# Optimization experiments

Hardware: AMD Instinct MI355X
Metric: run time of the kernel (lower is better)

## Reference

```python
import jax, jax.numpy as jnp
import numpy as np

N, E, IN, H, L = 100000, 1600000, 128, 64, 3


def setup_inputs() -> dict:
    key = jax.random.key(0)
    ks = jax.random.split(key, 4)
    x = jax.random.normal(ks[0], (N, IN), dtype=jnp.float32)
    edge_index = jax.random.randint(ks[1], (2, E), 0, N, dtype=jnp.int32)
    enc_w = jax.random.normal(ks[2], (IN, H), dtype=jnp.float32) * 0.05
    enc_b = jnp.zeros((H,), jnp.float32)
    conv_w = jax.random.normal(ks[3], (L, H, H), dtype=jnp.float32) * 0.05
    conv_b = jnp.zeros((L, H), jnp.float32)
    return {"x": x, "edge_index": edge_index, "enc_w": enc_w, "enc_b": enc_b,
            "conv_w": conv_w, "conv_b": conv_b}


def _nuc(m):
    # nuclear norm of [N, C] via eigvals of the small C x C Gram matrix
    g = m.T @ m
    ev = jnp.linalg.eigvalsh(g)
    return jnp.sum(jnp.sqrt(jnp.clip(ev, 0.0, None)))


def _rank_diff(x):
    xn = x / _nuc(x)
    i = jnp.argmax(jnp.sum(jnp.abs(xn), axis=1))
    j = jnp.argmax(jnp.sum(jnp.abs(xn), axis=0))
    m0 = jnp.take(xn, i, axis=0)[None, :]   # [1, C]
    m1 = jnp.take(xn, j, axis=1)[:, None]   # [N, 1]
    m0 = jnp.where(jnp.take(m0[0], j) < 0.0, -m0, m0)
    xh = m1 @ m0
    xh = xh / _nuc(xh)
    return _nuc(xn - xh)


def _dirichlet(x, src, dst, deg, rw):
    # edges (src, dst) already include self loops; deg = degree(src)
    xn = x / jnp.linalg.norm(x)
    if rw:
        d = xn[src] - xn[dst]
        e = jnp.sum(d * d)
    else:
        xs = xn * jax.lax.rsqrt(deg)[:, None]
        d = xs[src] - xs[dst]
        coef = jax.lax.rsqrt(deg[src] * deg[dst])
        e = jnp.sum(coef * jnp.sum(d * d, axis=1))
    return 0.5 * e


def reference(x, edge_index, enc_w, enc_b, conv_w, conv_b):
    n = x.shape[0]
    loops = jnp.arange(n, dtype=edge_index.dtype)
    src = jnp.concatenate([edge_index[0], loops])
    dst = jnp.concatenate([edge_index[1], loops])
    ones = jnp.ones(src.shape[0], x.dtype)
    deg_dst = jax.ops.segment_sum(ones, dst, num_segments=n)   # GCN norm degree
    dis = jax.lax.rsqrt(deg_dst)
    norm = dis[src] * dis[dst]
    deg_src = jax.ops.segment_sum(ones, src, num_segments=n)   # dirichlet degree

    h = x @ enc_w + enc_b                                      # encoder
    energies = [_dirichlet(jax.lax.stop_gradient(h), src, dst, deg_src, rw=False)]
    energies_sym = []
    ranks = []
    for i in range(L):
        # GCNConv: linear -> gather -> sym-normalized scatter-add -> bias
        xw = h @ conv_w[i]
        msg = xw[src] * norm[:, None]
        h = jax.ops.segment_sum(msg, dst, num_segments=n) + conv_b[i]
        h = jax.nn.relu(h)
        hs = jax.lax.stop_gradient(h)
        energies.append(_dirichlet(hs, src, dst, deg_src, rw=True))
        energies_sym.append(_dirichlet(hs, src, dst, deg_src, rw=False))
        ranks.append(_rank_diff(hs))
    return h, jnp.stack(energies), jnp.stack(energies_sym), jnp.stack(ranks)
```

## Files before the change

### kernel.cpp

```cpp
#include <hip/hip_runtime.h>

#define WF 64

__device__ inline float wredsum(float v) {
#pragma unroll
  for (int m = 32; m; m >>= 1) v += __shfl_xor(v, m, WF);
  return v;
}
__device__ inline float4 wredsum4(float4 v) {
#pragma unroll
  for (int m = 32; m; m >>= 1) {
    v.x += __shfl_xor(v.x, m, WF);
    v.y += __shfl_xor(v.y, m, WF);
    v.z += __shfl_xor(v.z, m, WF);
    v.w += __shfl_xor(v.w, m, WF);
  }
  return v;
}
__device__ inline float wredmin(float v) {
#pragma unroll
  for (int m = 32; m; m >>= 1) v = fminf(v, __shfl_xor(v, m, WF));
  return v;
}
__device__ inline float wredmax(float v) {
#pragma unroll
  for (int m = 32; m; m >>= 1) v = fmaxf(v, __shfl_xor(v, m, WF));
  return v;
}

__device__ inline float fastrcp(float x) {
  float r;
  asm("v_rcp_f32 %0, %1" : "=v"(r) : "v"(x));
  return r;
}

__device__ inline void atomAddF(float* p, float v) { unsafeAtomicAdd(p, v); }

__global__ __launch_bounds__(256) void k_init(int* degs, int* degd, float* G,
                                              float* colsum, float* scal, int n) {
  int i = blockIdx.x * 256 + threadIdx.x;
  if (i < n) { degs[i] = 1; degd[i] = 1; }
  if (i < 3 * 4096) G[i] = 0.f;
  if (i < 3 * 64) colsum[i] = 0.f;
  if (i < 64) scal[i] = 0.f;
}

__global__ __launch_bounds__(256) void k_deg(const int* src, const int* dst,
                                             int* degs, int* degd, int e) {
  int i = blockIdx.x * 256 + threadIdx.x;
  int stride = gridDim.x * 256;
  for (; i < e; i += stride) {
    atomicAdd(&degs[src[i]], 1);
    atomicAdd(&degd[dst[i]], 1);
  }
}

__global__ __launch_bounds__(256) void k_nodescal(const int* degs, const int* degd,
                                                  float4* cn4, float* degsum, int n) {
  int i = blockIdx.x * 256 + threadIdx.x;
  if (i < n) {
    float fs = (float)degs[i], fd = (float)degd[i];
    float rs_ = rsqrtf(fs);
    float4 v;
    v.x = rsqrtf(fd);
    v.y = 1.f / fs;
    v.z = rs_;
    v.w = rs_ * rs_ * rs_;
    cn4[i] = v;
    degsum[i] = fs + fd;
  }
}

__global__ __launch_bounds__(256) void k_scan1(const int* degd, int* start, int* bsum, int n) {
  __shared__ int sb[256];
  int t = threadIdx.x, i = blockIdx.x * 256 + t;
  int v = (i < n) ? degd[i] : 0;
  sb[t] = v;
  __syncthreads();
  for (int off = 1; off < 256; off <<= 1) {
    int add = (t >= off) ? sb[t - off] : 0;
    __syncthreads();
    sb[t] += add;
    __syncthreads();
  }
  if (i < n) start[i] = sb[t] - v;
  if (t == 255) bsum[blockIdx.x] = sb[255];
}

__global__ __launch_bounds__(512) void k_scan2(int* bsum, int nb) {
  __shared__ int sb[512];
  int t = threadIdx.x;
  int v = (t < nb) ? bsum[t] : 0;
  sb[t] = v;
  __syncthreads();
  for (int off = 1; off < 512; off <<= 1) {
    int add = (t >= off) ? sb[t - off] : 0;
    __syncthreads();
    sb[t] += add;
    __syncthreads();
  }
  if (t < nb) bsum[t] = sb[t] - v;
}

__global__ __launch_bounds__(256) void k_scan3(int* start, const int* bsum, int* cursor,
                                               int n, int total) {
  int i = blockIdx.x * 256 + threadIdx.x;
  if (i < n) {
    int v = start[i] + bsum[i >> 8];
    start[i] = v;
    cursor[i] = v;
  }
  if (i == 0) start[n] = total;
}

__global__ __launch_bounds__(256) void k_scatter(const int* src, const int* dst, int* cursor,
                                                 int* csr, int e, int n) {
  int i = blockIdx.x * 256 + threadIdx.x;
  int tot = e + n;
  if (i >= tot) return;
  int s, d;
  if (i < e) { s = src[i]; d = dst[i]; } else { s = i - e; d = i - e; }
  int pos = atomicAdd(&cursor[d], 1);
  csr[pos] = s;
}

__global__ __launch_bounds__(256) void k_enc(const float* __restrict__ x,
                                             const float* __restrict__ W,
                                             const float* __restrict__ b,
                                             const float4* __restrict__ cn4,
                                             float* __restrict__ X,
                                             float* __restrict__ nsq,
                                             float4* __restrict__ P, int n) {
  __shared__ float Wl[128 * 64];
  for (int idx = threadIdx.x; idx < 128 * 64; idx += 256) Wl[idx] = W[idx];
  __syncthreads();
  int w = threadIdx.x >> 6, c = threadIdx.x & 63;
  float bc = b[c];
  for (int node = blockIdx.x * 4 + w; node < n; node += gridDim.x * 4) {
    const float4* xr4 = (const float4*)(x + (size_t)node * 128);
    float acc = bc;
#pragma unroll
    for (int k4 = 0; k4 < 32; k4++) {
      float4 xv = xr4[k4];
      acc += xv.x * Wl[(k4 * 4 + 0) * 64 + c];
      acc += xv.y * Wl[(k4 * 4 + 1) * 64 + c];
      acc += xv.z * Wl[(k4 * 4 + 2) * 64 + c];
      acc += xv.w * Wl[(k4 * 4 + 3) * 64 + c];
    }
    X[(size_t)node * 64 + c] = acc;
    float r = wredsum(acc * acc);
    if (c == 0) {
      nsq[node] = r;
      float4 c4 = cn4[node];
      P[node] = make_float4(c4.x, c4.y, c4.z, r * c4.w);
    }
  }
}

template <int AGGC>
__device__ inline void gather4(const float* __restrict__ H, const float4* __restrict__ P,
                               const int* __restrict__ csr, int k0, int k1, int g, int l16,
                               float4& agg0, float4& agg1, float4& aggC,
                               float& su, float& sv) {
  int kk = k0 + g;
  int last = k1 - 1;
  int s0 = csr[min(kk, last)];
  int s1 = csr[min(kk + 4, last)];
  int s2 = csr[min(kk + 8, last)];
  int s3 = csr[min(kk + 12, last)];
  while (kk < k1) {
    int kn = kk + 16;
    float4 h0 = *(const float4*)(H + (size_t)s0 * 64 + 4 * l16);
    float4 h1 = *(const float4*)(H + (size_t)s1 * 64 + 4 * l16);
    float4 h2 = *(const float4*)(H + (size_t)s2 * 64 + 4 * l16);
    float4 h3 = *(const float4*)(H + (size_t)s3 * 64 + 4 * l16);
    float4 Q0 = P[s0], Q1 = P[s1], Q2 = P[s2], Q3 = P[s3];
    s0 = csr[min(kn, last)];
    s1 = csr[min(kn + 4, last)];
    s2 = csr[min(kn + 8, last)];
    s3 = csr[min(kn + 12, last)];
    float m1 = (kk + 4 < k1) ? 1.f : 0.f;
    float m2 = (kk + 8 < k1) ? 1.f : 0.f;
    float m3 = (kk + 12 < k1) ? 1.f : 0.f;
    agg0.x += h0.x; agg0.y += h0.y; agg0.z += h0.z; agg0.w += h0.w;
    agg1.x = fmaf(h0.x, Q0.y, agg1.x); agg1.y = fmaf(h0.y, Q0.y, agg1.y);
    agg1.z = fmaf(h0.z, Q0.y, agg1.z); agg1.w = fmaf(h0.w, Q0.y, agg1.w);
    if (AGGC) {
      aggC.x = fmaf(h0.x, Q0.x, aggC.x); aggC.y = fmaf(h0.y, Q0.x, aggC.y);
      aggC.z = fmaf(h0.z, Q0.x, aggC.z); aggC.w = fmaf(h0.w, Q0.x, aggC.w);
    }
    su += Q0.w; sv += Q0.z;
    {
      float y = Q1.y * m1;
      agg0.x = fmaf(h1.x, m1, agg0.x); agg0.y = fmaf(h1.y, m1, agg0.y);
      agg0.z = fmaf(h1.z, m1, agg0.z); agg0.w = fmaf(h1.w, m1, agg0.w);
      agg1.x = fmaf(h1.x, y, agg1.x); agg1.y = fmaf(h1.y, y, agg1.y);
      agg1.z = fmaf(h1.z, y, agg1.z); agg1.w = fmaf(h1.w, y, agg1.w);
      if (AGGC) {
        float xq = Q1.x * m1;
        aggC.x = fmaf(h1.x, xq, aggC.x); aggC.y = fmaf(h1.y, xq, aggC.y);
        aggC.z = fmaf(h1.z, xq, aggC.z); aggC.w = fmaf(h1.w, xq, aggC.w);
      }
      su = fmaf(Q1.w, m1, su); sv = fmaf(Q1.z, m1, sv);
    }
    {
      float y = Q2.y * m2;
      agg0.x = fmaf(h2.x, m2, agg0.x); agg0.y = fmaf(h2.y, m2, agg0.y);
      agg0.z = fmaf(h2.z, m2, agg0.z); agg0.w = fmaf(h2.w, m2, agg0.w);
      agg1.x = fmaf(h2.x, y, agg1.x); agg1.y = fmaf(h2.y, y, agg1.y);
      agg1.z = fmaf(h2.z, y, agg1.z); agg1.w = fmaf(h2.w, y, agg1.w);
      if (AGGC) {
        float xq = Q2.x * m2;
        aggC.x = fmaf(h2.x, xq, aggC.x); aggC.y = fmaf(h2.y, xq, aggC.y);
        aggC.z = fmaf(h2.z, xq, aggC.z); aggC.w = fmaf(h2.w, xq, aggC.w);
      }
      su = fmaf(Q2.w, m2, su); sv = fmaf(Q2.z, m2, sv);
    }
    {
      float y = Q3.y * m3;
      agg0.x = fmaf(h3.x, m3, agg0.x); agg0.y = fmaf(h3.y, m3, agg0.y);
      agg0.z = fmaf(h3.z, m3, agg0.z); agg0.w = fmaf(h3.w, m3, agg0.w);
      agg1.x = fmaf(h3.x, y, agg1.x); agg1.y = fmaf(h3.y, y, agg1.y);
      agg1.z = fmaf(h3.z, y, agg1.z); agg1.w = fmaf(h3.w, y, agg1.w);
      if (AGGC) {
        float xq = Q3.x * m3;
        aggC.x = fmaf(h3.x, xq, aggC.x); aggC.y = fmaf(h3.y, xq, aggC.y);
        aggC.z = fmaf(h3.z, xq, aggC.z); aggC.w = fmaf(h3.w, xq, aggC.w);
      }
      su = fmaf(Q3.w, m3, su); sv = fmaf(Q3.z, m3, sv);
    }
    kk = kn;
  }
}

__global__ __launch_bounds__(256) void k_convpass(
    const float* __restrict__ H, const float4* __restrict__ P,
    const float* __restrict__ nsq, const float* __restrict__ degsum,
    const float4* __restrict__ cn4, const int* __restrict__ start,
    const int* __restrict__ csr, const float* __restrict__ W,
    const float* __restrict__ bias, float* __restrict__ T,
    float4* __restrict__ Pn, float* __restrict__ nsqN,
    float* __restrict__ scal5, float* __restrict__ G, float* __restrict__ colsum,
    float* __restrict__ bmv, int* __restrict__ bmi, int n) {
  __shared__ float Wl[4096];
  __shared__ float rowbuf[4][64];
  __shared__ float red[4][5];
  __shared__ float colred[4][64];
  __shared__ float mvs[4];
  __shared__ int mis[4];
  int t = threadIdx.x, w = t >> 6, lane = t & 63, g = lane >> 4, l16 = lane & 15;
  for (int i = t; i < 4096; i += 256) Wl[i] = W[i];
  __syncthreads();
  float a0 = 0.f, a1 = 0.f, a2 = 0.f, a3 = 0.f, a4 = 0.f;
  float Greg[16];
#pragma unroll
  for (int k = 0; k < 16; k++) Greg[k] = 0.f;
  float cacc = 0.f, best = -1.f;
  int bi = 0;
  float bc = bias[lane];
  int wid = blockIdx.x * 4 + w, nw = gridDim.x * 4;
  int iters = (n + nw - 1) / nw;
  for (int it = 0; it < iters; it++) {
    int d = wid + it * nw;
    bool valid = d < n;
    float tv = 0.f;
    if (valid) {
      int k0 = start[d], k1 = start[d + 1];
      float4 hd = *(const float4*)(H + (size_t)d * 64 + 4 * l16);
      float4 pd = P[d];
      float nqd = nsq[d];
      float dsum = degsum[d];
      float4 agg0 = {0.f, 0.f, 0.f, 0.f};
      float4 agg1 = {0.f, 0.f, 0.f, 0.f};
      float4 aggC = {0.f, 0.f, 0.f, 0.f};
      float su = 0.f, sv = 0.f;
      gather4<1>(H, P, csr, k0, k1, g, l16, agg0, agg1, aggC, su, sv);
      float td0 = agg0.x * hd.x + agg0.y * hd.y + agg0.z * hd.z + agg0.w * hd.w;
      float td1 = agg1.x * hd.x + agg1.y * hd.y + agg1.z * hd.z + agg1.w * hd.w;
      float4 r4 = wredsum4(make_float4(td0, td1, su, sv));
      float dot1 = r4.x, dot2 = r4.y;
      su = r4.z * 0.0625f;
      sv = r4.w * 0.0625f;
      a0 += dsum * nqd;
      a1 += dot1;
      a2 += pd.z * su + pd.w * sv;
      a3 += pd.y * dot2;
      a4 += nqd;
      aggC.x += __shfl_xor(aggC.x, 16); aggC.y += __shfl_xor(aggC.y, 16);
      aggC.z += __shfl_xor(aggC.z, 16); aggC.w += __shfl_xor(aggC.w, 16);
      aggC.x += __shfl_xor(aggC.x, 32); aggC.y += __shfl_xor(aggC.y, 32);
      aggC.z += __shfl_xor(aggC.z, 32); aggC.w += __shfl_xor(aggC.w, 32);
      float mv = 0.f;
#pragma unroll
      for (int kq = 0; kq < 16; kq++) {
        float ax = __shfl(aggC.x, kq, 16);
        float ay = __shfl(aggC.y, kq, 16);
        float az = __shfl(aggC.z, kq, 16);
        float aw = __shfl(aggC.w, kq, 16);
        mv += ax * Wl[(4 * kq + 0) * 64 + lane];
        mv += ay * Wl[(4 * kq + 1) * 64 + lane];
        mv += az * Wl[(4 * kq + 2) * 64 + lane];
        mv += aw * Wl[(4 * kq + 3) * 64 + lane];
      }
      tv = fmaxf(fmaf(pd.x, mv, bc), 0.f);
      T[(size_t)d * 64 + lane] = tv;
      float r = wredsum(tv * tv);
      float atv = fabsf(tv);
      cacc += atv;
      float rsum = wredsum(atv);
      if (rsum > best) { best = rsum; bi = d; }
      if (lane == 0) {
        nsqN[d] = r;
        float4 c4 = cn4[d];
        Pn[d] = make_float4(c4.x, c4.y, c4.z, r * c4.w);
      }
    }
    rowbuf[w][lane] = tv;
    __syncthreads();
#pragma unroll
    for (int rr = 0; rr < 4; rr++) {
      float hj = rowbuf[rr][lane];
#pragma unroll
      for (int k = 0; k < 16; k++) Greg[k] = fmaf(rowbuf[rr][w + 4 * k], hj, Greg[k]);
    }
    __syncthreads();
  }
#pragma unroll
  for (int k = 0; k < 16; k++) atomAddF(&G[(w + 4 * k) * 64 + lane], Greg[k]);
  colred[w][lane] = cacc;
  if (lane == 0) {
    red[w][0] = a0; red[w][1] = a1; red[w][2] = a2; red[w][3] = a3; red[w][4] = a4;
    mvs[w] = best; mis[w] = bi;
  }
  __syncthreads();
  if (t < 64) {
    float cs = colred[0][t] + colred[1][t] + colred[2][t] + colred[3][t];
    atomAddF(&colsum[t], cs);
  }
  if (t == 0) {
#pragma unroll
    for (int j = 0; j < 5; j++)
      atomAddF(&scal5[j], red[0][j] + red[1][j] + red[2][j] + red[3][j]);
    float bv = mvs[0]; int bix = mis[0];
    for (int q = 1; q < 4; q++)
      if (mvs[q] > bv || (mvs[q] == bv && mis[q] < bix)) { bv = mvs[q]; bix = mis[q]; }
    bmv[blockIdx.x] = bv;
    bmi[blockIdx.x] = bix;
  }
}

__global__ __launch_bounds__(64) void k_finalize(const float* T, const float* bmv,
                                                 const int* bmi, int nblocks,
                                                 const float* colsum, float* rowslot,
                                                 int* jstar, int n) {
  int t = threadIdx.x;
  float bv = -1.f;
  int bix = 0x7fffffff;
  for (int b = t; b < nblocks; b += 64) {
    float v = bmv[b]; int ix = bmi[b];
    if (v > bv || (v == bv && ix < bix)) { bv = v; bix = ix; }
  }
#pragma unroll
  for (int m = 32; m; m >>= 1) {
    float ov = __shfl_xor(bv, m); int oi = __shfl_xor(bix, m);
    if (ov > bv || (ov == bv && oi < bix)) { bv = ov; bix = oi; }
  }
  float cv = colsum[t];
  int cj = t;
#pragma unroll
  for (int m = 32; m; m >>= 1) {
    float ov = __shfl_xor(cv, m); int oj = __shfl_xor(cj, m);
    if (ov > cv || (ov == cv && oj < cj)) { cv = ov; cj = oj; }
  }
  if (t == 0) jstar[0] = cj;
  rowslot[t] = T[(size_t)bix * 64 + t];
}

__device__ float tridiag_sumsqrt(float (*A)[65], float* vbuf, float* wbuf,
                                 float (*wpart)[64], float2* de, float* esh, int t) {
  bool w0 = (t < 64);
  int lane = t & 63, w4 = t >> 6;
  for (int k = 0; k < 62; k++) {
    float beta = 0.f;
    if (w0) {
      float acol = A[t][k];
      float xs = (t >= k + 2) ? acol : 0.f;
      float sigma = wredsum(xs * xs);
      float x1 = __shfl(acol, k + 1, WF);
      float alpha = -copysignf(sqrtf(fmaf(x1, x1, sigma)), x1);
      float v1 = x1 - alpha;
      float vv = fmaf(v1, v1, sigma);
      beta = (vv > 1e-37f) ? 2.f / vv : 0.f;
      vbuf[t] = (t == k + 1) ? v1 : xs;
      if (t == 0) esh[k] = alpha;
    }
    __syncthreads();
    {
      float s0 = 0.f, s1 = 0.f, s2 = 0.f, s3 = 0.f;
#pragma unroll
      for (int i2 = 0; i2 < 4; i2++) {
        int j = w4 + 16 * i2;
        s0 = fmaf(A[lane][j], vbuf[j], s0);
        s1 = fmaf(A[lane][j + 4], vbuf[j + 4], s1);
        s2 = fmaf(A[lane][j + 8], vbuf[j + 8], s2);
        s3 = fmaf(A[lane][j + 12], vbuf[j + 12], s3);
      }
      wpart[w4][lane] = (s0 + s1) + (s2 + s3);
    }
    __syncthreads();
    if (w0) {
      float p = beta * (wpart[0][t] + wpart[1][t] + wpart[2][t] + wpart[3][t]);
      float dot = wredsum(vbuf[t] * p);
      float K = 0.5f * beta * dot;
      wbuf[t] = fmaf(-K, vbuf[t], p);
    }
    __syncthreads();
    {
      float vj = vbuf[lane], wj = wbuf[lane];
#pragma unroll
      for (int i2 = 0; i2 < 16; i2++) {
        int i = w4 + 4 * i2;
        A[i][lane] -= vbuf[i] * wj + wbuf[i] * vj;
      }
    }
    __syncthreads();
  }
  if (t == 0) { esh[62] = A[63][62]; esh[63] = 0.f; }
  __syncthreads();
  float gmin = 0.f, gmax = 0.f;
  if (w0) {
    float dt = A[t][t];
    float ep = (t >= 1) ? esh[t - 1] : 0.f;
    float en = (t <= 62) ? esh[t] : 0.f;
    de[t] = make_float2(dt, ep * ep);
    float rad = fabsf(ep) + fabsf(en);
    gmin = wredmin(dt - rad);
    gmax = wredmax(dt + rad);
  }
  __syncthreads();
  float lam = 0.f;
  if (w0) {
    float range = gmax - gmin;
    float lo = gmin - 1e-3f * range - 1e-30f;
    float hi = gmax + 1e-3f * range + 1e-30f;
    for (int it = 0; it < 30; it++) {
      float mid = 0.5f * (lo + hi);
      float q = de[0].x - mid;
      int cnt = (q < 0.f) ? 1 : 0;
      for (int i = 1; i < 64; i++) {
        float2 dc = de[i];
        float qq = (dc.x - mid) - dc.y * fastrcp(q);
        q = (fabsf(qq) < 1e-30f) ? -1e-30f : qq;
        cnt += (q < 0.f) ? 1 : 0;
      }
      if (cnt > t) hi = mid; else lo = mid;
    }
    lam = 0.5f * (lo + hi);
  }
  float svv = w0 ? sqrtf(fmaxf(lam, 0.f)) : 0.f;
  return wredsum(svv);
}

__global__ __launch_bounds__(256, 4) void k_final(
    const float* __restrict__ H, const float4* __restrict__ P,
    const float* __restrict__ nsq, const float* __restrict__ degsum,
    const int* __restrict__ start, const int* __restrict__ csr,
    float* __restrict__ scal5, const float* __restrict__ Gbase,
    const float* __restrict__ rowslot, const int* __restrict__ jstar,
    float* __restrict__ rankOut, int n, int nbE) {
  __shared__ float A[64][65];
  __shared__ float vbuf[64], wbuf[64], esh[64];
  __shared__ float wpart[4][64];
  __shared__ float2 de[64];
  __shared__ float u[64], m0[64];
  __shared__ float shn;
  __shared__ float red[4][5];
  int t = threadIdx.x, w = t >> 6, lane = t & 63, g = lane >> 4, l16 = lane & 15;
  if (blockIdx.x < 3) {
    int l = blockIdx.x;
    const float* Gl = Gbase + l * 4096;
    for (int idx = t; idx < 4096; idx += 256) A[idx >> 6][idx & 63] = Gl[idx];
    __syncthreads();
    float nuc1 = tridiag_sumsqrt(A, vbuf, wbuf, wpart, de, esh, t);
    if (t == 0) shn = nuc1;
    __syncthreads();
    float s = 1.f / shn;
    int js = jstar[l];
    if (t < 64) {
      float rv = rowslot[l * 64 + t];
      float rn2 = wredsum(rv * rv);
      float sign = (rowslot[l * 64 + js] < 0.f) ? -1.f : 1.f;
      m0[t] = sign * rv * rsqrtf(rn2);
      u[t] = s * Gl[t * 64 + js] * rsqrtf(Gl[js * 64 + js]);
    }
    __syncthreads();
    float s2 = s * s;
    for (int idx = t; idx < 4096; idx += 256) {
      int i = idx >> 6, j = idx & 63;
      A[i][j] = s2 * Gl[idx] - u[i] * m0[j] - m0[i] * u[j] + m0[i] * m0[j];
    }
    __syncthreads();
    float nuc2 = tridiag_sumsqrt(A, vbuf, wbuf, wpart, de, esh, t);
    if (t == 0) rankOut[l] = nuc2;
    return;
  }
  float a0 = 0.f, a1 = 0.f, a2 = 0.f, a3 = 0.f, a4 = 0.f;
  int wid = (blockIdx.x - 3) * 4 + w, nw = nbE * 4;
  for (int d = wid; d < n; d += nw) {
    int k0 = start[d], k1 = start[d + 1];
    float4 hd = *(const float4*)(H + (size_t)d * 64 + 4 * l16);
    float4 pd = P[d];
    float nqd = nsq[d];
    float dsum = degsum[d];
    float4 agg0 = {0.f, 0.f, 0.f, 0.f};
    float4 agg1 = {0.f, 0.f, 0.f, 0.f};
    float4 aggC = {0.f, 0.f, 0.f, 0.f};
    float su = 0.f, sv = 0.f;
    gather4<0>(H, P, csr, k0, k1, g, l16, agg0, agg1, aggC, su, sv);
    float td0 = agg0.x * hd.x + agg0.y * hd.y + agg0.z * hd.z + agg0.w * hd.w;
    float td1 = agg1.x * hd.x + agg1.y * hd.y + agg1.z * hd.z + agg1.w * hd.w;
    float4 r4 = wredsum4(make_float4(td0, td1, su, sv));
    a0 += dsum * nqd;
    a1 += r4.x;
    a2 += pd.z * (r4.z * 0.0625f) + pd.w * (r4.w * 0.0625f);
    a3 += pd.y * r4.y;
    a4 += nqd;
  }
  if (lane == 0) {
    red[w][0] = a0; red[w][1] = a1; red[w][2] = a2; red[w][3] = a3; red[w][4] = a4;
  }
  __syncthreads();
  if (t == 0) {
#pragma unroll
    for (int j = 0; j < 5; j++)
      atomAddF(&scal5[j], red[0][j] + red[1][j] + red[2][j] + red[3][j]);
  }
}

__global__ __launch_bounds__(64) void k_epi(const float* scal, float* outsc) {
  if (threadIdx.x == 0) {
    for (int st = 0; st < 4; st++) {
      const float* a = scal + 5 * st;
      float inv = 1.f / a[4];
      float rw = 0.5f * (a[0] - 2.f * a[1]) * inv;
      float sym = 0.5f * (a[2] - 2.f * a[3]) * inv;
      if (st == 0) outsc[0] = sym;
      else { outsc[st] = rw; outsc[3 + st] = sym; }
    }
    for (int l = 0; l < 3; l++) outsc[7 + l] = scal[20 + l];
  }
}

extern "C" void kernel_launch(void* const* d_in, const int* in_sizes, int n_in,
                              void* d_out, int out_size, void* d_ws, size_t ws_size,
                              hipStream_t stream) {
  const float* x      = (const float*)d_in[0];
  const int*   ei     = (const int*)d_in[1];
  const float* enc_w  = (const float*)d_in[2];
  const float* enc_b  = (const float*)d_in[3];
  const float* conv_w = (const float*)d_in[4];
  const float* conv_b = (const float*)d_in[5];
  const int n = in_sizes[0] / 128;
  const int e = in_sizes[1] / 2;
  const int* src = ei;
  const int* dst = ei + e;
  float* OUT = (float*)d_out;
  float* outsc = OUT + (size_t)n * 64;

  char* p = (char*)d_ws;
  auto alloc = [&](size_t bytes) -> char* {
    char* r = p;
    p += (bytes + 255) & ~size_t(255);
    return r;
  };
  float*  X      = (float*)alloc((size_t)n * 64 * 4);
  float*  Yf     = (float*)alloc((size_t)n * 64 * 4);
  int*    csr    = (int*)alloc((size_t)(e + n) * 4);
  int*    degs   = (int*)alloc((size_t)n * 4);
  int*    degd   = (int*)alloc((size_t)n * 4);
  float4* cn4    = (float4*)alloc((size_t)n * 16);
  float*  degsum = (float*)alloc((size_t)n * 4);
  int*    start  = (int*)alloc((size_t)(n + 1) * 4);
  int*    cursor = (int*)alloc((size_t)n * 4);
  int*    bsum   = (int*)alloc(4096);
  float*  nsqA   = (float*)alloc((size_t)n * 4);
  float*  nsqB   = (float*)alloc((size_t)n * 4);
  float4* Pa     = (float4*)alloc((size_t)n * 16);
  float4* Pb     = (float4*)alloc((size_t)n * 16);
  float*  G      = (float*)alloc(3 * 4096 * 4);
  float*  colsum = (float*)alloc(3 * 64 * 4);
  float*  bmv    = (float*)alloc(2048 * 4);
  int*    bmi    = (int*)alloc(2048 * 4);
  float*  rowslot= (float*)alloc(3 * 64 * 4);
  float*  scal   = (float*)alloc(64 * 4);
  int*    ij     = (int*)alloc(64 * 4);

  int nb = (n + 255) / 256;
  const int NBL = 2048;

  k_init<<<nb, 256, 0, stream>>>(degs, degd, G, colsum, scal, n);
  k_deg<<<2048, 256, 0, stream>>>(src, dst, degs, degd, e);
  k_nodescal<<<nb, 256, 0, stream>>>(degs, degd, cn4, degsum, n);
  k_scan1<<<nb, 256, 0, stream>>>(degd, start, bsum, n);
  k_scan2<<<1, 512, 0, stream>>>(bsum, nb);
  k_scan3<<<nb, 256, 0, stream>>>(start, bsum, cursor, n, e + n);
  k_scatter<<<(e + n + 255) / 256, 256, 0, stream>>>(src, dst, cursor, csr, e, n);
  k_enc<<<NBL, 256, 0, stream>>>(x, enc_w, enc_b, cn4, X, nsqA, Pa, n);

  k_convpass<<<NBL, 256, 0, stream>>>(X, Pa, nsqA, degsum, cn4, start, csr,
                                      conv_w, conv_b, Yf, Pb, nsqB,
                                      scal, G, colsum, bmv, bmi, n);
  k_finalize<<<1, 64, 0, stream>>>(Yf, bmv, bmi, NBL, colsum, rowslot, ij, n);

  k_convpass<<<NBL, 256, 0, stream>>>(Yf, Pb, nsqB, degsum, cn4, start, csr,
                                      conv_w + 4096, conv_b + 64, X, Pa, nsqA,
                                      scal + 5, G + 4096, colsum + 64, bmv, bmi, n);
  k_finalize<<<1, 64, 0, stream>>>(X, bmv, bmi, NBL, colsum + 64, rowslot + 64, ij + 1, n);

  k_convpass<<<NBL, 256, 0, stream>>>(X, Pa, nsqA, degsum, cn4, start, csr,
                                      conv_w + 2 * 4096, conv_b + 128, OUT, Pb, nsqB,
                                      scal + 10, G + 2 * 4096, colsum + 128, bmv, bmi, n);
  k_finalize<<<1, 64, 0, stream>>>(OUT, bmv, bmi, NBL, colsum + 128, rowslot + 128, ij + 2, n);

  k_final<<<NBL + 3, 256, 0, stream>>>(OUT, Pb, nsqB, degsum, start, csr,
                                       scal + 15, G, rowslot, ij, scal + 20, n, NBL);
  k_epi<<<1, 64, 0, stream>>>(scal, outsc);
}
```

Measured before the change: 1.435 ms.

## Gather neighbor features in bf16, shrink per-node scalars, overlap rank solves with conv passes

```diff
diff --git a/kernel.cpp b/kernel.cpp
--- a/kernel.cpp
+++ b/kernel.cpp
@@ -35,6 +35,36 @@
 }
 
 __device__ inline void atomAddF(float* p, float v) { unsafeAtomicAdd(p, v); }
+
+__device__ inline unsigned short f2bf(float f) {
+  unsigned u = __float_as_uint(f);
+  unsigned r = u + 0x7FFFu + ((u >> 16) & 1u);
+  return (unsigned short)(r >> 16);
+}
+__device__ inline float bf2f(unsigned short h) {
+  return __uint_as_float(((unsigned)h) << 16);
+}
+
+struct ConvS {
+  float Wl[4096];
+  float rowbuf[4][64];
+  float red[4][5];
+  float colred[4][64];
+  float mvs[4];
+  int mis[4];
+};
+struct RankS {
+  float A[64][65];
+  float vbuf[64], wbuf[64], esh[64];
+  float wpart[4][64];
+  float2 de[64];
+  float u[64], m0[64];
+  float shn;
+};
+union SmemU {
+  ConvS c;
+  RankS r;
+};
 
 __global__ __launch_bounds__(256) void k_init(int* degs, int* degd, float* G,
                                               float* colsum, float* scal, int n) {
@@ -56,17 +86,11 @@
 }
 
 __global__ __launch_bounds__(256) void k_nodescal(const int* degs, const int* degd,
-                                                  float4* cn4, float* degsum, int n) {
+                                                  float2* Pf, float* degsum, int n) {
   int i = blockIdx.x * 256 + threadIdx.x;
   if (i < n) {
     float fs = (float)degs[i], fd = (float)degd[i];
-    float rs_ = rsqrtf(fs);
-    float4 v;
-    v.x = rsqrtf(fd);
-    v.y = 1.f / fs;
-    v.z = rs_;
-    v.w = rs_ * rs_ * rs_;
-    cn4[i] = v;
+    Pf[i] = make_float2(rsqrtf(fd), rsqrtf(fs));
     degsum[i] = fs + fd;
   }
 }
@@ -127,10 +151,9 @@
 __global__ __launch_bounds__(256) void k_enc(const float* __restrict__ x,
                                              const float* __restrict__ W,
                                              const float* __restrict__ b,
-                                             const float4* __restrict__ cn4,
                                              float* __restrict__ X,
-                                             float* __restrict__ nsq,
-                                             float4* __restrict__ P, int n) {
+                                             unsigned short* __restrict__ Xb,
+                                             float* __restrict__ nsq, int n) {
   __shared__ float Wl[128 * 64];
   for (int idx = threadIdx.x; idx < 128 * 64; idx += 256) Wl[idx] = W[idx];
   __syncthreads();
@@ -148,17 +171,15 @@
       acc += xv.w * Wl[(k4 * 4 + 3) * 64 + c];
     }
     X[(size_t)node * 64 + c] = acc;
+    Xb[(size_t)node * 64 + c] = f2bf(acc);
     float r = wredsum(acc * acc);
-    if (c == 0) {
-      nsq[node] = r;
-      float4 c4 = cn4[node];
-      P[node] = make_float4(c4.x, c4.y, c4.z, r * c4.w);
-    }
+    if (c == 0) nsq[node] = r;
   }
 }
 
 template <int AGGC>
-__device__ inline void gather4(const float* __restrict__ H, const float4* __restrict__ P,
+__device__ inline void gatherB(const unsigned short* __restrict__ Hb,
+                               const float2* __restrict__ Pf,
                                const int* __restrict__ csr, int k0, int k1, int g, int l16,
                                float4& agg0, float4& agg1, float4& aggC,
                                float& su, float& sv) {
@@ -170,11 +191,11 @@
   int s3 = csr[min(kk + 12, last)];
   while (kk < k1) {
     int kn = kk + 16;
-    float4 h0 = *(const float4*)(H + (size_t)s0 * 64 + 4 * l16);
-    float4 h1 = *(const float4*)(H + (size_t)s1 * 64 + 4 * l16);
-    float4 h2 = *(const float4*)(H + (size_t)s2 * 64 + 4 * l16);
-    float4 h3 = *(const float4*)(H + (size_t)s3 * 64 + 4 * l16);
-    float4 Q0 = P[s0], Q1 = P[s1], Q2 = P[s2], Q3 = P[s3];
+    ushort4 b0 = *(const ushort4*)(Hb + (size_t)s0 * 64 + 4 * l16);
+    ushort4 b1 = *(const ushort4*)(Hb + (size_t)s1 * 64 + 4 * l16);
+    ushort4 b2 = *(const ushort4*)(Hb + (size_t)s2 * 64 + 4 * l16);
+    ushort4 b3 = *(const ushort4*)(Hb + (size_t)s3 * 64 + 4 * l16);
+    float2 p0 = Pf[s0], p1 = Pf[s1], p2 = Pf[s2], p3 = Pf[s3];
     s0 = csr[min(kn, last)];
     s1 = csr[min(kn + 4, last)];
     s2 = csr[min(kn + 8, last)];
@@ -182,74 +203,204 @@
     float m1 = (kk + 4 < k1) ? 1.f : 0.f;
     float m2 = (kk + 8 < k1) ? 1.f : 0.f;
     float m3 = (kk + 12 < k1) ? 1.f : 0.f;
-    agg0.x += h0.x; agg0.y += h0.y; agg0.z += h0.z; agg0.w += h0.w;
-    agg1.x = fmaf(h0.x, Q0.y, agg1.x); agg1.y = fmaf(h0.y, Q0.y, agg1.y);
-    agg1.z = fmaf(h0.z, Q0.y, agg1.z); agg1.w = fmaf(h0.w, Q0.y, agg1.w);
-    if (AGGC) {
-      aggC.x = fmaf(h0.x, Q0.x, aggC.x); aggC.y = fmaf(h0.y, Q0.x, aggC.y);
-      aggC.z = fmaf(h0.z, Q0.x, aggC.z); aggC.w = fmaf(h0.w, Q0.x, aggC.w);
-    }
-    su += Q0.w; sv += Q0.z;
     {
-      float y = Q1.y * m1;
-      agg0.x = fmaf(h1.x, m1, agg0.x); agg0.y = fmaf(h1.y, m1, agg0.y);
-      agg0.z = fmaf(h1.z, m1, agg0.z); agg0.w = fmaf(h1.w, m1, agg0.w);
-      agg1.x = fmaf(h1.x, y, agg1.x); agg1.y = fmaf(h1.y, y, agg1.y);
-      agg1.z = fmaf(h1.z, y, agg1.z); agg1.w = fmaf(h1.w, y, agg1.w);
+      float hx = bf2f(b0.x), hy = bf2f(b0.y), hz = bf2f(b0.z), hw = bf2f(b0.w);
+      float rs = p0.y, dis = p0.x;
+      float y = rs * rs, q3 = y * rs;
+      agg0.x += hx; agg0.y += hy; agg0.z += hz; agg0.w += hw;
+      agg1.x = fmaf(hx, y, agg1.x); agg1.y = fmaf(hy, y, agg1.y);
+      agg1.z = fmaf(hz, y, agg1.z); agg1.w = fmaf(hw, y, agg1.w);
       if (AGGC) {
-        float xq = Q1.x * m1;
-        aggC.x = fmaf(h1.x, xq, aggC.x); aggC.y = fmaf(h1.y, xq, aggC.y);
-        aggC.z = fmaf(h1.z, xq, aggC.z); aggC.w = fmaf(h1.w, xq, aggC.w);
-      }
-      su = fmaf(Q1.w, m1, su); sv = fmaf(Q1.z, m1, sv);
+        aggC.x = fmaf(hx, dis, aggC.x); aggC.y = fmaf(hy, dis, aggC.y);
+        aggC.z = fmaf(hz, dis, aggC.z); aggC.w = fmaf(hw, dis, aggC.w);
+      }
+      float d2 = fmaf(hx, hx, fmaf(hy, hy, fmaf(hz, hz, hw * hw)));
+      su = fmaf(q3, d2, su);
+      sv += rs;
     }
     {
-      float y = Q2.y * m2;
-      agg0.x = fmaf(h2.x, m2, agg0.x); agg0.y = fmaf(h2.y, m2, agg0.y);
-      agg0.z = fmaf(h2.z, m2, agg0.z); agg0.w = fmaf(h2.w, m2, agg0.w);
-      agg1.x = fmaf(h2.x, y, agg1.x); agg1.y = fmaf(h2.y, y, agg1.y);
-      agg1.z = fmaf(h2.z, y, agg1.z); agg1.w = fmaf(h2.w, y, agg1.w);
+      float hx = bf2f(b1.x), hy = bf2f(b1.y), hz = bf2f(b1.z), hw = bf2f(b1.w);
+      float rs = p1.y * m1, dis = p1.x * m1;
+      float y = rs * rs, q3 = y * rs;
+      agg0.x = fmaf(hx, m1, agg0.x); agg0.y = fmaf(hy, m1, agg0.y);
+      agg0.z = fmaf(hz, m1, agg0.z); agg0.w = fmaf(hw, m1, agg0.w);
+      agg1.x = fmaf(hx, y, agg1.x); agg1.y = fmaf(hy, y, agg1.y);
+      agg1.z = fmaf(hz, y, agg1.z); agg1.w = fmaf(hw, y, agg1.w);
       if (AGGC) {
-        float xq = Q2.x * m2;
-        aggC.x = fmaf(h2.x, xq, aggC.x); aggC.y = fmaf(h2.y, xq, aggC.y);
-        aggC.z = fmaf(h2.z, xq, aggC.z); aggC.w = fmaf(h2.w, xq, aggC.w);
-      }
-      su = fmaf(Q2.w, m2, su); sv = fmaf(Q2.z, m2, sv);
+        aggC.x = fmaf(hx, dis, aggC.x); aggC.y = fmaf(hy, dis, aggC.y);
+        aggC.z = fmaf(hz, dis, aggC.z); aggC.w = fmaf(hw, dis, aggC.w);
+      }
+      float d2 = fmaf(hx, hx, fmaf(hy, hy, fmaf(hz, hz, hw * hw)));
+      su = fmaf(q3, d2, su);
+      sv += rs;
     }
     {
-      float y = Q3.y * m3;
-      agg0.x = fmaf(h3.x, m3, agg0.x); agg0.y = fmaf(h3.y, m3, agg0.y);
-      agg0.z = fmaf(h3.z, m3, agg0.z); agg0.w = fmaf(h3.w, m3, agg0.w);
-      agg1.x = fmaf(h3.x, y, agg1.x); agg1.y = fmaf(h3.y, y, agg1.y);
-      agg1.z = fmaf(h3.z, y, agg1.z); agg1.w = fmaf(h3.w, y, agg1.w);
+      float hx = bf2f(b2.x), hy = bf2f(b2.y), hz = bf2f(b2.z), hw = bf2f(b2.w);
+      float rs = p2.y * m2, dis = p2.x * m2;
+      float y = rs * rs, q3 = y * rs;
+      agg0.x = fmaf(hx, m2, agg0.x); agg0.y = fmaf(hy, m2, agg0.y);
+      agg0.z = fmaf(hz, m2, agg0.z); agg0.w = fmaf(hw, m2, agg0.w);
+      agg1.x = fmaf(hx, y, agg1.x); agg1.y = fmaf(hy, y, agg1.y);
+      agg1.z = fmaf(hz, y, agg1.z); agg1.w = fmaf(hw, y, agg1.w);
       if (AGGC) {
-        float xq = Q3.x * m3;
-        aggC.x = fmaf(h3.x, xq, aggC.x); aggC.y = fmaf(h3.y, xq, aggC.y);
-        aggC.z = fmaf(h3.z, xq, aggC.z); aggC.w = fmaf(h3.w, xq, aggC.w);
-      }
-      su = fmaf(Q3.w, m3, su); sv = fmaf(Q3.z, m3, sv);
+        aggC.x = fmaf(hx, dis, aggC.x); aggC.y = fmaf(hy, dis, aggC.y);
+        aggC.z = fmaf(hz, dis, aggC.z); aggC.w = fmaf(hw, dis, aggC.w);
+      }
+      float d2 = fmaf(hx, hx, fmaf(hy, hy, fmaf(hz, hz, hw * hw)));
+      su = fmaf(q3, d2, su);
+      sv += rs;
+    }
+    {
+      float hx = bf2f(b3.x), hy = bf2f(b3.y), hz = bf2f(b3.z), hw = bf2f(b3.w);
+      float rs = p3.y * m3, dis = p3.x * m3;
+      float y = rs * rs, q3 = y * rs;
+      agg0.x = fmaf(hx, m3, agg0.x); agg0.y = fmaf(hy, m3, agg0.y);
+      agg0.z = fmaf(hz, m3, agg0.z); agg0.w = fmaf(hw, m3, agg0.w);
+      agg1.x = fmaf(hx, y, agg1.x); agg1.y = fmaf(hy, y, agg1.y);
+      agg1.z = fmaf(hz, y, agg1.z); agg1.w = fmaf(hw, y, agg1.w);
+      if (AGGC) {
+        aggC.x = fmaf(hx, dis, aggC.x); aggC.y = fmaf(hy, dis, aggC.y);
+        aggC.z = fmaf(hz, dis, aggC.z); aggC.w = fmaf(hw, dis, aggC.w);
+      }
+      float d2 = fmaf(hx, hx, fmaf(hy, hy, fmaf(hz, hz, hw * hw)));
+      su = fmaf(q3, d2, su);
+      sv += rs;
     }
     kk = kn;
   }
 }
 
+__device__ float tridiag_sumsqrt(RankS& S, int t) {
+  bool w0 = (t < 64);
+  int lane = t & 63, w4 = t >> 6;
+  for (int k = 0; k < 62; k++) {
+    float beta = 0.f;
+    if (w0) {
+      float acol = S.A[t][k];
+      float xs = (t >= k + 2) ? acol : 0.f;
+      float sigma = wredsum(xs * xs);
+      float x1 = __shfl(acol, k + 1, WF);
+      float alpha = -copysignf(sqrtf(fmaf(x1, x1, sigma)), x1);
+      float v1 = x1 - alpha;
+      float vv = fmaf(v1, v1, sigma);
+      beta = (vv > 1e-37f) ? 2.f / vv : 0.f;
+      S.vbuf[t] = (t == k + 1) ? v1 : xs;
+      if (t == 0) S.esh[k] = alpha;
+    }
+    __syncthreads();
+    {
+      float s0 = 0.f, s1 = 0.f, s2 = 0.f, s3 = 0.f;
+#pragma unroll
+      for (int i2 = 0; i2 < 4; i2++) {
+        int j = w4 + 16 * i2;
+        s0 = fmaf(S.A[lane][j], S.vbuf[j], s0);
+        s1 = fmaf(S.A[lane][j + 4], S.vbuf[j + 4], s1);
+        s2 = fmaf(S.A[lane][j + 8], S.vbuf[j + 8], s2);
+        s3 = fmaf(S.A[lane][j + 12], S.vbuf[j + 12], s3);
+      }
+      S.wpart[w4][lane] = (s0 + s1) + (s2 + s3);
+    }
+    __syncthreads();
+    if (w0) {
+      float p = beta * (S.wpart[0][t] + S.wpart[1][t] + S.wpart[2][t] + S.wpart[3][t]);
+      float dot = wredsum(S.vbuf[t] * p);
+      float K = 0.5f * beta * dot;
+      S.wbuf[t] = fmaf(-K, S.vbuf[t], p);
+    }
+    __syncthreads();
+    {
+      float vj = S.vbuf[lane], wj = S.wbuf[lane];
+#pragma unroll
+      for (int i2 = 0; i2 < 16; i2++) {
+        int i = w4 + 4 * i2;
+        S.A[i][lane] -= S.vbuf[i] * wj + S.wbuf[i] * vj;
+      }
+    }
+    __syncthreads();
+  }
+  if (t == 0) { S.esh[62] = S.A[63][62]; S.esh[63] = 0.f; }
+  __syncthreads();
+  float gmin = 0.f, gmax = 0.f;
+  if (w0) {
+    float dt = S.A[t][t];
+    float ep = (t >= 1) ? S.esh[t - 1] : 0.f;
+    float en = (t <= 62) ? S.esh[t] : 0.f;
+    S.de[t] = make_float2(dt, ep * ep);
+    float rad = fabsf(ep) + fabsf(en);
+    gmin = wredmin(dt - rad);
+    gmax = wredmax(dt + rad);
+  }
+  __syncthreads();
+  float lam = 0.f;
+  if (w0) {
+    float range = gmax - gmin;
+    float lo = gmin - 1e-3f * range - 1e-30f;
+    float hi = gmax + 1e-3f * range + 1e-30f;
+    for (int it = 0; it < 30; it++) {
+      float mid = 0.5f * (lo + hi);
+      float q = S.de[0].x - mid;
+      int cnt = (q < 0.f) ? 1 : 0;
+      for (int i = 1; i < 64; i++) {
+        float2 dc = S.de[i];
+        float qq = (dc.x - mid) - dc.y * fastrcp(q);
+        q = (fabsf(qq) < 1e-30f) ? -1e-30f : qq;
+        cnt += (q < 0.f) ? 1 : 0;
+      }
+      if (cnt > t) hi = mid; else lo = mid;
+    }
+    lam = 0.5f * (lo + hi);
+  }
+  float svv = w0 ? sqrtf(fmaxf(lam, 0.f)) : 0.f;
+  return wredsum(svv);
+}
+
+__device__ void rank_block(RankS& S, const float* __restrict__ Gl,
+                           const float* __restrict__ rowslot_l,
+                           const int* __restrict__ jstar_l,
+                           float* __restrict__ rankOut_l, int t) {
+  for (int idx = t; idx < 4096; idx += 256) S.A[idx >> 6][idx & 63] = Gl[idx];
+  __syncthreads();
+  float nuc1 = tridiag_sumsqrt(S, t);
+  if (t == 0) S.shn = nuc1;
+  __syncthreads();
+  float s = 1.f / S.shn;
+  int js = jstar_l[0];
+  if (t < 64) {
+    float rv = rowslot_l[t];
+    float rn2 = wredsum(rv * rv);
+    float sign = (rowslot_l[js] < 0.f) ? -1.f : 1.f;
+    S.m0[t] = sign * rv * rsqrtf(rn2);
+    S.u[t] = s * Gl[t * 64 + js] * rsqrtf(Gl[js * 64 + js]);
+  }
+  __syncthreads();
+  float s2 = s * s;
+  for (int idx = t; idx < 4096; idx += 256) {
+    int i = idx >> 6, j = idx & 63;
+    S.A[i][j] = s2 * Gl[idx] - S.u[i] * S.m0[j] - S.m0[i] * S.u[j] + S.m0[i] * S.m0[j];
+  }
+  __syncthreads();
+  float nuc2 = tridiag_sumsqrt(S, t);
+  if (t == 0) rankOut_l[0] = nuc2;
+}
+
 __global__ __launch_bounds__(256) void k_convpass(
-    const float* __restrict__ H, const float4* __restrict__ P,
-    const float* __restrict__ nsq, const float* __restrict__ degsum,
-    const float4* __restrict__ cn4, const int* __restrict__ start,
+    const float* __restrict__ H, const unsigned short* __restrict__ Hb,
+    const float2* __restrict__ Pf, const float* __restrict__ nsq,
+    const float* __restrict__ degsum, const int* __restrict__ start,
     const int* __restrict__ csr, const float* __restrict__ W,
     const float* __restrict__ bias, float* __restrict__ T,
-    float4* __restrict__ Pn, float* __restrict__ nsqN,
+    unsigned short* __restrict__ Tb, float* __restrict__ nsqN,
     float* __restrict__ scal5, float* __restrict__ G, float* __restrict__ colsum,
-    float* __restrict__ bmv, int* __restrict__ bmi, int n) {
-  __shared__ float Wl[4096];
-  __shared__ float rowbuf[4][64];
-  __shared__ float red[4][5];
-  __shared__ float colred[4][64];
-  __shared__ float mvs[4];
-  __shared__ int mis[4];
+    float* __restrict__ bmv, int* __restrict__ bmi, int n, int nbC,
+    const float* __restrict__ Gr, const float* __restrict__ rowslotR,
+    const int* __restrict__ jstarR, float* __restrict__ rankOutR) {
+  __shared__ SmemU sm;
   int t = threadIdx.x, w = t >> 6, lane = t & 63, g = lane >> 4, l16 = lane & 15;
-  for (int i = t; i < 4096; i += 256) Wl[i] = W[i];
+  if (blockIdx.x >= nbC) {
+    rank_block(sm.r, Gr, rowslotR, jstarR, rankOutR, t);
+    return;
+  }
+  for (int i = t; i < 4096; i += 256) sm.c.Wl[i] = W[i];
   __syncthreads();
   float a0 = 0.f, a1 = 0.f, a2 = 0.f, a3 = 0.f, a4 = 0.f;
   float Greg[16];
@@ -258,7 +409,7 @@
   float cacc = 0.f, best = -1.f;
   int bi = 0;
   float bc = bias[lane];
-  int wid = blockIdx.x * 4 + w, nw = gridDim.x * 4;
+  int wid = blockIdx.x * 4 + w, nw = nbC * 4;
   int iters = (n + nw - 1) / nw;
   for (int it = 0; it < iters; it++) {
     int d = wid + it * nw;
@@ -267,24 +418,24 @@
     if (valid) {
       int k0 = start[d], k1 = start[d + 1];
       float4 hd = *(const float4*)(H + (size_t)d * 64 + 4 * l16);
-      float4 pd = P[d];
+      float2 pfd = Pf[d];
       float nqd = nsq[d];
       float dsum = degsum[d];
       float4 agg0 = {0.f, 0.f, 0.f, 0.f};
       float4 agg1 = {0.f, 0.f, 0.f, 0.f};
       float4 aggC = {0.f, 0.f, 0.f, 0.f};
       float su = 0.f, sv = 0.f;
-      gather4<1>(H, P, csr, k0, k1, g, l16, agg0, agg1, aggC, su, sv);
+      gatherB<1>(Hb, Pf, csr, k0, k1, g, l16, agg0, agg1, aggC, su, sv);
       float td0 = agg0.x * hd.x + agg0.y * hd.y + agg0.z * hd.z + agg0.w * hd.w;
       float td1 = agg1.x * hd.x + agg1.y * hd.y + agg1.z * hd.z + agg1.w * hd.w;
       float4 r4 = wredsum4(make_float4(td0, td1, su, sv));
-      float dot1 = r4.x, dot2 = r4.y;
+      float rsd = pfd.y;
       su = r4.z * 0.0625f;
       sv = r4.w * 0.0625f;
       a0 += dsum * nqd;
-      a1 += dot1;
-      a2 += pd.z * su + pd.w * sv;
-      a3 += pd.y * dot2;
+      a1 += r4.x;
+      a2 += rsd * su + nqd * (rsd * rsd * rsd) * sv;
+      a3 += (rsd * rsd) * r4.y;
       a4 += nqd;
       aggC.x += __shfl_xor(aggC.x, 16); aggC.y += __shfl_xor(aggC.y, 16);
       aggC.z += __shfl_xor(aggC.z, 16); aggC.w += __shfl_xor(aggC.w, 16);
@@ -297,53 +448,53 @@
         float ay = __shfl(aggC.y, kq, 16);
         float az = __shfl(aggC.z, kq, 16);
         float aw = __shfl(aggC.w, kq, 16);
-        mv += ax * Wl[(4 * kq + 0) * 64 + lane];
-        mv += ay * Wl[(4 * kq + 1) * 64 + lane];
-        mv += az * Wl[(4 * kq + 2) * 64 + lane];
-        mv += aw * Wl[(4 * kq + 3) * 64 + lane];
-      }
-      tv = fmaxf(fmaf(pd.x, mv, bc), 0.f);
+        mv += ax * sm.c.Wl[(4 * kq + 0) * 64 + lane];
+        mv += ay * sm.c.Wl[(4 * kq + 1) * 64 + lane];
+        mv += az * sm.c.Wl[(4 * kq + 2) * 64 + lane];
+        mv += aw * sm.c.Wl[(4 * kq + 3) * 64 + lane];
+      }
+      tv = fmaxf(fmaf(pfd.x, mv, bc), 0.f);
       T[(size_t)d * 64 + lane] = tv;
+      Tb[(size_t)d * 64 + lane] = f2bf(tv);
       float r = wredsum(tv * tv);
       float atv = fabsf(tv);
       cacc += atv;
       float rsum = wredsum(atv);
       if (rsum > best) { best = rsum; bi = d; }
-      if (lane == 0) {
-        nsqN[d] = r;
-        float4 c4 = cn4[d];
-        Pn[d] = make_float4(c4.x, c4.y, c4.z, r * c4.w);
-      }
-    }
-    rowbuf[w][lane] = tv;
+      if (lane == 0) nsqN[d] = r;
+    }
+    sm.c.rowbuf[w][lane] = tv;
     __syncthreads();
 #pragma unroll
     for (int rr = 0; rr < 4; rr++) {
-      float hj = rowbuf[rr][lane];
-#pragma unroll
-      for (int k = 0; k < 16; k++) Greg[k] = fmaf(rowbuf[rr][w + 4 * k], hj, Greg[k]);
+      float hj = sm.c.rowbuf[rr][lane];
+#pragma unroll
+      for (int k = 0; k < 16; k++) Greg[k] = fmaf(sm.c.rowbuf[rr][w + 4 * k], hj, Greg[k]);
     }
     __syncthreads();
   }
 #pragma unroll
   for (int k = 0; k < 16; k++) atomAddF(&G[(w + 4 * k) * 64 + lane], Greg[k]);
-  colred[w][lane] = cacc;
+  sm.c.colred[w][lane] = cacc;
   if (lane == 0) {
-    red[w][0] = a0; red[w][1] = a1; red[w][2] = a2; red[w][3] = a3; red[w][4] = a4;
-    mvs[w] = best; mis[w] = bi;
+    sm.c.red[w][0] = a0; sm.c.red[w][1] = a1; sm.c.red[w][2] = a2;
+    sm.c.red[w][3] = a3; sm.c.red[w][4] = a4;
+    sm.c.mvs[w] = best; sm.c.mis[w] = bi;
   }
   __syncthreads();
   if (t < 64) {
-    float cs = colred[0][t] + colred[1][t] + colred[2][t] + colred[3][t];
+    float cs = sm.c.colred[0][t] + sm.c.colred[1][t] + sm.c.colred[2][t] + sm.c.colred[3][t];
     atomAddF(&colsum[t], cs);
   }
   if (t == 0) {
 #pragma unroll
     for (int j = 0; j < 5; j++)
-      atomAddF(&scal5[j], red[0][j] + red[1][j] + red[2][j] + red[3][j]);
-    float bv = mvs[0]; int bix = mis[0];
+      atomAddF(&scal5[j], sm.c.red[0][j] + sm.c.red[1][j] + sm.c.red[2][j] + sm.c.red[3][j]);
+    float bv = sm.c.mvs[0]; int bix = sm.c.mis[0];
     for (int q = 1; q < 4; q++)
-      if (mvs[q] > bv || (mvs[q] == bv && mis[q] < bix)) { bv = mvs[q]; bix = mis[q]; }
+      if (sm.c.mvs[q] > bv || (sm.c.mvs[q] == bv && sm.c.mis[q] < bix)) {
+        bv = sm.c.mvs[q]; bix = sm.c.mis[q];
+      }
     bmv[blockIdx.x] = bv;
     bmi[blockIdx.x] = bix;
   }
@@ -376,164 +527,51 @@
   rowslot[t] = T[(size_t)bix * 64 + t];
 }
 
-__device__ float tridiag_sumsqrt(float (*A)[65], float* vbuf, float* wbuf,
-                                 float (*wpart)[64], float2* de, float* esh, int t) {
-  bool w0 = (t < 64);
-  int lane = t & 63, w4 = t >> 6;
-  for (int k = 0; k < 62; k++) {
-    float beta = 0.f;
-    if (w0) {
-      float acol = A[t][k];
-      float xs = (t >= k + 2) ? acol : 0.f;
-      float sigma = wredsum(xs * xs);
-      float x1 = __shfl(acol, k + 1, WF);
-      float alpha = -copysignf(sqrtf(fmaf(x1, x1, sigma)), x1);
-      float v1 = x1 - alpha;
-      float vv = fmaf(v1, v1, sigma);
-      beta = (vv > 1e-37f) ? 2.f / vv : 0.f;
-      vbuf[t] = (t == k + 1) ? v1 : xs;
-      if (t == 0) esh[k] = alpha;
-    }
-    __syncthreads();
-    {
-      float s0 = 0.f, s1 = 0.f, s2 = 0.f, s3 = 0.f;
-#pragma unroll
-      for (int i2 = 0; i2 < 4; i2++) {
-        int j = w4 + 16 * i2;
-        s0 = fmaf(A[lane][j], vbuf[j], s0);
-        s1 = fmaf(A[lane][j + 4], vbuf[j + 4], s1);
-        s2 = fmaf(A[lane][j + 8], vbuf[j + 8], s2);
-        s3 = fmaf(A[lane][j + 12], vbuf[j + 12], s3);
-      }
-      wpart[w4][lane] = (s0 + s1) + (s2 + s3);
-    }
-    __syncthreads();
-    if (w0) {
-      float p = beta * (wpart[0][t] + wpart[1][t] + wpart[2][t] + wpart[3][t]);
-      float dot = wredsum(vbuf[t] * p);
-      float K = 0.5f * beta * dot;
-      wbuf[t] = fmaf(-K, vbuf[t], p);
-    }
-    __syncthreads();
-    {
-      float vj = vbuf[lane], wj = wbuf[lane];
-#pragma unroll
-      for (int i2 = 0; i2 < 16; i2++) {
-        int i = w4 + 4 * i2;
-        A[i][lane] -= vbuf[i] * wj + wbuf[i] * vj;
-      }
-    }
-    __syncthreads();
-  }
-  if (t == 0) { esh[62] = A[63][62]; esh[63] = 0.f; }
-  __syncthreads();
-  float gmin = 0.f, gmax = 0.f;
-  if (w0) {
-    float dt = A[t][t];
-    float ep = (t >= 1) ? esh[t - 1] : 0.f;
-    float en = (t <= 62) ? esh[t] : 0.f;
-    de[t] = make_float2(dt, ep * ep);
-    float rad = fabsf(ep) + fabsf(en);
-    gmin = wredmin(dt - rad);
-    gmax = wredmax(dt + rad);
-  }
-  __syncthreads();
-  float lam = 0.f;
-  if (w0) {
-    float range = gmax - gmin;
-    float lo = gmin - 1e-3f * range - 1e-30f;
-    float hi = gmax + 1e-3f * range + 1e-30f;
-    for (int it = 0; it < 30; it++) {
-      float mid = 0.5f * (lo + hi);
-      float q = de[0].x - mid;
-      int cnt = (q < 0.f) ? 1 : 0;
-      for (int i = 1; i < 64; i++) {
-        float2 dc = de[i];
-        float qq = (dc.x - mid) - dc.y * fastrcp(q);
-        q = (fabsf(qq) < 1e-30f) ? -1e-30f : qq;
-        cnt += (q < 0.f) ? 1 : 0;
-      }
-      if (cnt > t) hi = mid; else lo = mid;
-    }
-    lam = 0.5f * (lo + hi);
-  }
-  float svv = w0 ? sqrtf(fmaxf(lam, 0.f)) : 0.f;
-  return wredsum(svv);
-}
-
-__global__ __launch_bounds__(256, 4) void k_final(
-    const float* __restrict__ H, const float4* __restrict__ P,
-    const float* __restrict__ nsq, const float* __restrict__ degsum,
-    const int* __restrict__ start, const int* __restrict__ csr,
-    float* __restrict__ scal5, const float* __restrict__ Gbase,
-    const float* __restrict__ rowslot, const int* __restrict__ jstar,
-    float* __restrict__ rankOut, int n, int nbE) {
-  __shared__ float A[64][65];
-  __shared__ float vbuf[64], wbuf[64], esh[64];
-  __shared__ float wpart[4][64];
-  __shared__ float2 de[64];
-  __shared__ float u[64], m0[64];
-  __shared__ float shn;
-  __shared__ float red[4][5];
+__global__ __launch_bounds__(256) void k_final(
+    const float* __restrict__ H, const unsigned short* __restrict__ Hb,
+    const float2* __restrict__ Pf, const float* __restrict__ nsq,
+    const float* __restrict__ degsum, const int* __restrict__ start,
+    const int* __restrict__ csr, float* __restrict__ scal5,
+    const float* __restrict__ Gr, const float* __restrict__ rowslotR,
+    const int* __restrict__ jstarR, float* __restrict__ rankOutR, int n, int nbE) {
+  __shared__ SmemU sm;
   int t = threadIdx.x, w = t >> 6, lane = t & 63, g = lane >> 4, l16 = lane & 15;
-  if (blockIdx.x < 3) {
-    int l = blockIdx.x;
-    const float* Gl = Gbase + l * 4096;
-    for (int idx = t; idx < 4096; idx += 256) A[idx >> 6][idx & 63] = Gl[idx];
-    __syncthreads();
-    float nuc1 = tridiag_sumsqrt(A, vbuf, wbuf, wpart, de, esh, t);
-    if (t == 0) shn = nuc1;
-    __syncthreads();
-    float s = 1.f / shn;
-    int js = jstar[l];
-    if (t < 64) {
-      float rv = rowslot[l * 64 + t];
-      float rn2 = wredsum(rv * rv);
-      float sign = (rowslot[l * 64 + js] < 0.f) ? -1.f : 1.f;
-      m0[t] = sign * rv * rsqrtf(rn2);
-      u[t] = s * Gl[t * 64 + js] * rsqrtf(Gl[js * 64 + js]);
-    }
-    __syncthreads();
-    float s2 = s * s;
-    for (int idx = t; idx < 4096; idx += 256) {
-      int i = idx >> 6, j = idx & 63;
-      A[i][j] = s2 * Gl[idx] - u[i] * m0[j] - m0[i] * u[j] + m0[i] * m0[j];
-    }
-    __syncthreads();
-    float nuc2 = tridiag_sumsqrt(A, vbuf, wbuf, wpart, de, esh, t);
-    if (t == 0) rankOut[l] = nuc2;
+  if (blockIdx.x == 0) {
+    rank_block(sm.r, Gr, rowslotR, jstarR, rankOutR, t);
     return;
   }
   float a0 = 0.f, a1 = 0.f, a2 = 0.f, a3 = 0.f, a4 = 0.f;
-  int wid = (blockIdx.x - 3) * 4 + w, nw = nbE * 4;
+  int wid = (blockIdx.x - 1) * 4 + w, nw = nbE * 4;
   for (int d = wid; d < n; d += nw) {
     int k0 = start[d], k1 = start[d + 1];
     float4 hd = *(const float4*)(H + (size_t)d * 64 + 4 * l16);
-    float4 pd = P[d];
+    float2 pfd = Pf[d];
     float nqd = nsq[d];
     float dsum = degsum[d];
     float4 agg0 = {0.f, 0.f, 0.f, 0.f};
     float4 agg1 = {0.f, 0.f, 0.f, 0.f};
     float4 aggC = {0.f, 0.f, 0.f, 0.f};
     float su = 0.f, sv = 0.f;
-    gather4<0>(H, P, csr, k0, k1, g, l16, agg0, agg1, aggC, su, sv);
+    gatherB<0>(Hb, Pf, csr, k0, k1, g, l16, agg0, agg1, aggC, su, sv);
     float td0 = agg0.x * hd.x + agg0.y * hd.y + agg0.z * hd.z + agg0.w * hd.w;
     float td1 = agg1.x * hd.x + agg1.y * hd.y + agg1.z * hd.z + agg1.w * hd.w;
     float4 r4 = wredsum4(make_float4(td0, td1, su, sv));
+    float rsd = pfd.y;
     a0 += dsum * nqd;
     a1 += r4.x;
-    a2 += pd.z * (r4.z * 0.0625f) + pd.w * (r4.w * 0.0625f);
-    a3 += pd.y * r4.y;
+    a2 += rsd * (r4.z * 0.0625f) + nqd * (rsd * rsd * rsd) * (r4.w * 0.0625f);
+    a3 += (rsd * rsd) * r4.y;
     a4 += nqd;
   }
   if (lane == 0) {
-    red[w][0] = a0; red[w][1] = a1; red[w][2] = a2; red[w][3] = a3; red[w][4] = a4;
+    sm.c.red[w][0] = a0; sm.c.red[w][1] = a1; sm.c.red[w][2] = a2;
+    sm.c.red[w][3] = a3; sm.c.red[w][4] = a4;
   }
   __syncthreads();
   if (t == 0) {
 #pragma unroll
     for (int j = 0; j < 5; j++)
-      atomAddF(&scal5[j], red[0][j] + red[1][j] + red[2][j] + red[3][j]);
+      atomAddF(&scal5[j], sm.c.red[0][j] + sm.c.red[1][j] + sm.c.red[2][j] + sm.c.red[3][j]);
   }
 }
 
@@ -573,56 +611,61 @@
     p += (bytes + 255) & ~size_t(255);
     return r;
   };
-  float*  X      = (float*)alloc((size_t)n * 64 * 4);
-  float*  Yf     = (float*)alloc((size_t)n * 64 * 4);
-  int*    csr    = (int*)alloc((size_t)(e + n) * 4);
-  int*    degs   = (int*)alloc((size_t)n * 4);
-  int*    degd   = (int*)alloc((size_t)n * 4);
-  float4* cn4    = (float4*)alloc((size_t)n * 16);
-  float*  degsum = (float*)alloc((size_t)n * 4);
-  int*    start  = (int*)alloc((size_t)(n + 1) * 4);
-  int*    cursor = (int*)alloc((size_t)n * 4);
-  int*    bsum   = (int*)alloc(4096);
-  float*  nsqA   = (float*)alloc((size_t)n * 4);
-  float*  nsqB   = (float*)alloc((size_t)n * 4);
-  float4* Pa     = (float4*)alloc((size_t)n * 16);
-  float4* Pb     = (float4*)alloc((size_t)n * 16);
-  float*  G      = (float*)alloc(3 * 4096 * 4);
-  float*  colsum = (float*)alloc(3 * 64 * 4);
-  float*  bmv    = (float*)alloc(2048 * 4);
-  int*    bmi    = (int*)alloc(2048 * 4);
-  float*  rowslot= (float*)alloc(3 * 64 * 4);
-  float*  scal   = (float*)alloc(64 * 4);
-  int*    ij     = (int*)alloc(64 * 4);
+  float*          X      = (float*)alloc((size_t)n * 64 * 4);
+  float*          Yf     = (float*)alloc((size_t)n * 64 * 4);
+  unsigned short* Xb     = (unsigned short*)alloc((size_t)n * 64 * 2);
+  unsigned short* Ybb    = (unsigned short*)alloc((size_t)n * 64 * 2);
+  unsigned short* OUTb   = (unsigned short*)alloc((size_t)n * 64 * 2);
+  int*            csr    = (int*)alloc((size_t)(e + n) * 4);
+  int*            degs   = (int*)alloc((size_t)n * 4);
+  int*            degd   = (int*)alloc((size_t)n * 4);
+  float2*         Pf2    = (float2*)alloc((size_t)n * 8);
+  float*          degsum = (float*)alloc((size_t)n * 4);
+  int*            start  = (int*)alloc((size_t)(n + 1) * 4);
+  int*            cursor = (int*)alloc((size_t)n * 4);
+  int*            bsum   = (int*)alloc(4096);
+  float*          nsqA   = (float*)alloc((size_t)n * 4);
+  float*          nsqB   = (float*)alloc((size_t)n * 4);
+  float*          G      = (float*)alloc(3 * 4096 * 4);
+  float*          colsum = (float*)alloc(3 * 64 * 4);
+  float*          bmv    = (float*)alloc(2048 * 4);
+  int*            bmi    = (int*)alloc(2048 * 4);
+  float*          rowslot= (float*)alloc(3 * 64 * 4);
+  float*          scal   = (float*)alloc(64 * 4);
+  int*            ij     = (int*)alloc(64 * 4);
 
   int nb = (n + 255) / 256;
   const int NBL = 2048;
 
   k_init<<<nb, 256, 0, stream>>>(degs, degd, G, colsum, scal, n);
   k_deg<<<2048, 256, 0, stream>>>(src, dst, degs, degd, e);
-  k_nodescal<<<nb, 256, 0, stream>>>(degs, degd, cn4, degsum, n);
+  k_nodescal<<<nb, 256, 0, stream>>>(degs, degd, Pf2, degsum, n);
   k_scan1<<<nb, 256, 0, stream>>>(degd, start, bsum, n);
   k_scan2<<<1, 512, 0, stream>>>(bsum, nb);
   k_scan3<<<nb, 256, 0, stream>>>(start, bsum, cursor, n, e + n);
   k_scatter<<<(e + n + 255) / 256, 256, 0, stream>>>(src, dst, cursor, csr, e, n);
-  k_enc<<<NBL, 256, 0, stream>>>(x, enc_w, enc_b, cn4, X, nsqA, Pa, n);
-
-  k_convpass<<<NBL, 256, 0, stream>>>(X, Pa, nsqA, degsum, cn4, start, csr,
-                                      conv_w, conv_b, Yf, Pb, nsqB,
-                                      scal, G, colsum, bmv, bmi, n);
+  k_enc<<<NBL, 256, 0, stream>>>(x, enc_w, enc_b, X, Xb, nsqA, n);
+
+  k_convpass<<<NBL, 256, 0, stream>>>(X, Xb, Pf2, nsqA, degsum, start, csr,
+                                      conv_w, conv_b, Yf, Ybb, nsqB,
+                                      scal, G, colsum, bmv, bmi, n, NBL,
+                                      nullptr, nullptr, nullptr, nullptr);
   k_finalize<<<1, 64, 0, stream>>>(Yf, bmv, bmi, NBL, colsum, rowslot, ij, n);
 
-  k_convpass<<<NBL, 256, 0, stream>>>(Yf, Pb, nsqB, degsum, cn4, start, csr,
-                                      conv_w + 4096, conv_b + 64, X, Pa, nsqA,
-                                      scal + 5, G + 4096, colsum + 64, bmv, bmi, n);
+  k_convpass<<<NBL + 1, 256, 0, stream>>>(Yf, Ybb, Pf2, nsqB, degsum, start, csr,
+                                          conv_w + 4096, conv_b + 64, X, Xb, nsqA,
+                                          scal + 5, G + 4096, colsum + 64, bmv, bmi, n, NBL,
+                                          G, rowslot, ij, scal + 20);
   k_finalize<<<1, 64, 0, stream>>>(X, bmv, bmi, NBL, colsum + 64, rowslot + 64, ij + 1, n);
 
-  k_convpass<<<NBL, 256, 0, stream>>>(X, Pa, nsqA, degsum, cn4, start, csr,
-                                      conv_w + 2 * 4096, conv_b + 128, OUT, Pb, nsqB,
-                                      scal + 10, G + 2 * 4096, colsum + 128, bmv, bmi, n);
+  k_convpass<<<NBL + 1, 256, 0, stream>>>(X, Xb, Pf2, nsqA, degsum, start, csr,
+                                          conv_w + 2 * 4096, conv_b + 128, OUT, OUTb, nsqB,
+                                          scal + 10, G + 2 * 4096, colsum + 128, bmv, bmi, n, NBL,
+                                          G + 4096, rowslot + 64, ij + 1, scal + 21);
   k_finalize<<<1, 64, 0, stream>>>(OUT, bmv, bmi, NBL, colsum + 128, rowslot + 128, ij + 2, n);
 
-  k_final<<<NBL + 3, 256, 0, stream>>>(OUT, Pb, nsqB, degsum, start, csr,
-                                       scal + 15, G, rowslot, ij, scal + 20, n, NBL);
+  k_final<<<NBL + 1, 256, 0, stream>>>(OUT, OUTb, Pf2, nsqB, degsum, start, csr,
+                                       scal + 15, G + 2 * 4096, rowslot + 128, ij + 2,
+                                       scal + 22, n, NBL);
   k_epi<<<1, 64, 0, stream>>>(scal, outsc);
 }
```

Result: slower. 1.963 ms (+36.8%).
